# Kernel tuning notes

Measured on AMD Instinct MI355X. Metric: run time of the kernel, lower is better.

The kernel has to match this reference:

```python
import jax, jax.numpy as jnp
import numpy as np
from jax import lax

EPS = 1e-5
K = 32
S1, S2 = 512, 256


def bn_relu(x, gamma, beta, axes):
    # BatchNorm in training mode (batch statistics, biased variance) + ReLU.
    mean = jnp.mean(x, axis=axes, keepdims=True)
    var = jnp.var(x, axis=axes, keepdims=True)
    return jax.nn.relu((x - mean) * lax.rsqrt(var + EPS) * gamma + beta)


def fps(xyz, s):
    # Farthest point sampling, deterministic start at index 0. xyz: [N,3] -> [s] indices
    N = xyz.shape[0]
    def body(carry, _):
        dist, far = carry
        d = jnp.sum((xyz - xyz[far]) ** 2, axis=-1)
        dist = jnp.minimum(dist, d)
        return (dist, jnp.argmax(dist).astype(jnp.int32)), far
    init = (jnp.full((N,), 1e10, xyz.dtype), jnp.int32(0))
    _, idx = lax.scan(body, init, None, length=s)
    return idx


def sample_and_knn_group(s, k, coords, features):
    # coords: [B,N,3], features: [B,N,D]
    fps_idx = jax.vmap(lambda c: fps(c, s))(coords)                      # [B,s]
    new_xyz = jnp.take_along_axis(coords, fps_idx[..., None], axis=1)   # [B,s,3]
    new_feat = jnp.take_along_axis(features, fps_idx[..., None], axis=1)  # [B,s,D]
    # squared euclidean distances [B,s,N]
    d2 = (jnp.sum(new_xyz ** 2, -1)[..., None]
          - 2.0 * jnp.einsum('bsc,bnc->bsn', new_xyz, coords)
          + jnp.sum(coords ** 2, -1)[:, None, :])
    _, knn_idx = lax.top_k(-d2, k)                                       # [B,s,k]
    grouped = jax.vmap(lambda f, i: f[i])(features, knn_idx)             # [B,s,k,D]
    rel = grouped - new_feat[:, :, None, :]
    agg = jnp.concatenate([rel, jnp.broadcast_to(new_feat[:, :, None, :], rel.shape)], axis=-1)  # [B,s,k,2D]
    return new_xyz, agg


def sg_block(s, coords, feats, w1, cb1, g1, b1, w2, cb2, g2, b2):
    new_xyz, agg = sample_and_knn_group(s, K, coords, feats)
    h = bn_relu(jnp.einsum('bskc,oc->bsko', agg, w1) + cb1, g1, b1, (0, 1, 2))
    h = bn_relu(jnp.einsum('bskc,oc->bsko', h, w2) + cb2, g2, b2, (0, 1, 2))
    return new_xyz, jnp.max(h, axis=2)  # max over k neighbors -> [B,s,O]


def setup_inputs() -> dict:
    key = jax.random.key(0)
    ks = jax.random.split(key, 8)
    B, N = 16, 2048
    sc = 0.05
    return {
        'x': jax.random.normal(ks[0], (B, 3, N), jnp.float32),
        'emb_w1': jax.random.normal(ks[1], (64, 3), jnp.float32) * sc,
        'emb_g1': jnp.ones((64,), jnp.float32), 'emb_b1': jnp.zeros((64,), jnp.float32),
        'emb_w2': jax.random.normal(ks[2], (64, 64), jnp.float32) * sc,
        'emb_g2': jnp.ones((64,), jnp.float32), 'emb_b2': jnp.zeros((64,), jnp.float32),
        'sg1_w1': jax.random.normal(ks[3], (128, 128), jnp.float32) * sc,
        'sg1_cb1': jnp.zeros((128,), jnp.float32),
        'sg1_g1': jnp.ones((128,), jnp.float32), 'sg1_b1': jnp.zeros((128,), jnp.float32),
        'sg1_w2': jax.random.normal(ks[4], (128, 128), jnp.float32) * sc,
        'sg1_cb2': jnp.zeros((128,), jnp.float32),
        'sg1_g2': jnp.ones((128,), jnp.float32), 'sg1_b2': jnp.zeros((128,), jnp.float32),
        'sg2_w1': jax.random.normal(ks[5], (512, 256), jnp.float32) * sc,
        'sg2_cb1': jnp.zeros((512,), jnp.float32),
        'sg2_g1': jnp.ones((512,), jnp.float32), 'sg2_b1': jnp.zeros((512,), jnp.float32),
        'sg2_w2': jax.random.normal(ks[6], (512, 512), jnp.float32) * sc,
        'sg2_cb2': jnp.zeros((512,), jnp.float32),
        'sg2_g2': jnp.ones((512,), jnp.float32), 'sg2_b2': jnp.zeros((512,), jnp.float32),
    }


def reference(x, emb_w1, emb_g1, emb_b1, emb_w2, emb_g2, emb_b2,
              sg1_w1, sg1_cb1, sg1_g1, sg1_b1, sg1_w2, sg1_cb2, sg1_g2, sg1_b2,
              sg2_w1, sg2_cb1, sg2_g1, sg2_b1, sg2_w2, sg2_cb2, sg2_g2, sg2_b2):
    xyz = jnp.transpose(x, (0, 2, 1))  # [B,N,3]
    f = bn_relu(jnp.einsum('bnc,oc->bno', xyz, emb_w1), emb_g1, emb_b1, (0, 1))   # [B,N,64]
    f = bn_relu(jnp.einsum('bnc,oc->bno', f, emb_w2), emb_g2, emb_b2, (0, 1))
    xyz1, f1 = sg_block(S1, xyz, f, sg1_w1, sg1_cb1, sg1_g1, sg1_b1,
                        sg1_w2, sg1_cb2, sg1_g2, sg1_b2)   # [B,512,128]
    _, f2 = sg_block(S2, xyz1, f1, sg2_w1, sg2_cb1, sg2_g1, sg2_b1,
                     sg2_w2, sg2_cb2, sg2_g2, sg2_b2)      # [B,256,512]
    return jnp.transpose(f2, (0, 2, 1))  # [B,512,256] to match torch [B,C,s]
```

## Files before the change

kernel.cpp:

```cpp
#include <hip/hip_runtime.h>
#include <hip/hip_bf16.h>

#define EPS_BN 1e-5f
constexpr int BB = 16, NN = 2048, SS1 = 512, SS2 = 256, KNb = 32;

typedef short bf16x8 __attribute__((ext_vector_type(8)));
typedef float f32x4 __attribute__((ext_vector_type(4)));

__device__ inline float bflo(unsigned u) { return __uint_as_float(u << 16); }
__device__ inline float bfhi(unsigned u) { return __uint_as_float(u & 0xffff0000u); }
__device__ inline unsigned short f2bf_bits(float v) {
  __hip_bfloat16 h = __float2bfloat16(v);
  return *reinterpret_cast<unsigned short*>(&h);
}
__device__ inline unsigned fmono(float v) {
  int b = __float_as_int(v);
  return (unsigned)(b ^ ((b >> 31) | 0x80000000));
}
__device__ inline unsigned bn2(unsigned u, float s0, float h0, float s1, float h1) {
  float v0 = fmaxf(bflo(u) * s0 + h0, 0.f);
  float v1 = fmaxf(bfhi(u) * s1 + h1, 0.f);
  return (unsigned)f2bf_bits(v0) | ((unsigned)f2bf_bits(v1) << 16);
}

template <int CTRL>
__device__ inline void dpp_step_min(unsigned& hi, unsigned& lo) {
  unsigned hs = (unsigned)__builtin_amdgcn_update_dpp((int)hi, (int)hi, CTRL, 0xF, 0xF, false);
  unsigned ls = (unsigned)__builtin_amdgcn_update_dpp((int)lo, (int)lo, CTRL, 0xF, 0xF, false);
  bool take = (hs < hi) || (hs == hi && ls < lo);
  hi = take ? hs : hi; lo = take ? ls : lo;
}
template <int CTRL>
__device__ inline void dpp_step_maxv_minidx(unsigned& hi, unsigned& lo) {
  unsigned hs = (unsigned)__builtin_amdgcn_update_dpp((int)hi, (int)hi, CTRL, 0xF, 0xF, false);
  unsigned ls = (unsigned)__builtin_amdgcn_update_dpp((int)lo, (int)lo, CTRL, 0xF, 0xF, false);
  bool take = (hs > hi) || (hs == hi && ls < lo);
  hi = take ? hs : hi; lo = take ? ls : lo;
}
__device__ inline void dpp_chain_min(unsigned& hi, unsigned& lo) {
  dpp_step_min<0x111>(hi, lo); dpp_step_min<0x112>(hi, lo);
  dpp_step_min<0x114>(hi, lo); dpp_step_min<0x118>(hi, lo);
  dpp_step_min<0x142>(hi, lo); dpp_step_min<0x143>(hi, lo);
}
__device__ inline void dpp_chain_maxv_minidx(unsigned& hi, unsigned& lo) {
  dpp_step_maxv_minidx<0x111>(hi, lo); dpp_step_maxv_minidx<0x112>(hi, lo);
  dpp_step_maxv_minidx<0x114>(hi, lo); dpp_step_maxv_minidx<0x118>(hi, lo);
  dpp_step_maxv_minidx<0x142>(hi, lo); dpp_step_maxv_minidx<0x143>(hi, lo);
}
__device__ inline int dpp_reduce_min_idx(unsigned hi, unsigned lo) {
  dpp_chain_min(hi, lo);
  return __builtin_amdgcn_readlane((int)lo, 63);
}

__global__ __launch_bounds__(256, 1) void k_mega1(
    const float* __restrict__ x, const float* __restrict__ emb_w1,
    float* __restrict__ fA, double* __restrict__ rsE1, double* __restrict__ rqE1,
    int* __restrict__ fps1, float* __restrict__ nx1,
    int* __restrict__ fps2, float* __restrict__ nx2,
    const float* __restrict__ w11f, __hip_bfloat16* __restrict__ wb11,
    const float* __restrict__ w12f, __hip_bfloat16* __restrict__ wb12,
    const float* __restrict__ w21f, __hip_bfloat16* __restrict__ wb21,
    const float* __restrict__ w22f, __hip_bfloat16* __restrict__ wb22) {
  int blk = blockIdx.x;
  int t = threadIdx.x;
  if (blk < BB) {
    constexpr int PPL = NN / 256;
    int b = blk; int w = t >> 6; int lane = t & 63;
    __shared__ float4 sxyz[NN];
    __shared__ float4 c4[SS1];
    __shared__ unsigned combH[2][4], combL[2][4];
    float px[PPL], py[PPL], pz[PPL], ds[PPL];
#pragma unroll
    for (int r = 0; r < PPL; r++) {
      int i = r * 256 + t;
      float xx = x[(size_t)(b * 3 + 0) * NN + i];
      float yy = x[(size_t)(b * 3 + 1) * NN + i];
      float zz = x[(size_t)(b * 3 + 2) * NN + i];
      px[r] = xx; py[r] = yy; pz[r] = zz;
      float ox = xx, oy = yy, oz = zz;
      asm volatile("" : "+v"(ox), "+v"(oy), "+v"(oz));
      float4 o4 = {ox, oy, oz, 0.f};
      sxyz[i] = o4;
      ds[r] = 1e10f;
    }
    __syncthreads();
    int far = 0; int p = 0;
    for (int it = 0; it < SS1; it++) {
      float4 f4 = sxyz[far];
      float fx = f4.x, fy = f4.y, fz = f4.z;
      if (t == 0) {
        fps1[b * SS1 + it] = far;
        size_t ob = ((size_t)b * SS1 + it) * 3;
        nx1[ob] = fx; nx1[ob + 1] = fy; nx1[ob + 2] = fz;
        c4[it] = f4;
      }
      float mm0 = -1.f, mm1 = -1.f, mm2 = -1.f, mm3 = -1.f;
#pragma unroll
      for (int r = 0; r < PPL; r++) {
        float dx = px[r] - fx, dy = py[r] - fy, dz = pz[r] - fz;
        float d = dx * dx + dy * dy + dz * dz;
        float nd = d < ds[r] ? d : ds[r];
        ds[r] = nd;
        if ((r & 3) == 0) mm0 = nd > mm0 ? nd : mm0;
        else if ((r & 3) == 1) mm1 = nd > mm1 ? nd : mm1;
        else if ((r & 3) == 2) mm2 = nd > mm2 ? nd : mm2;
        else mm3 = nd > mm3 ? nd : mm3;
      }
      float m = fmaxf(fmaxf(mm0, mm1), fmaxf(mm2, mm3));
      int cand[PPL];
#pragma unroll
      for (int r = 0; r < PPL; r++) cand[r] = (ds[r] == m) ? (r * 256 + t) : 0x7fffffff;
#pragma unroll
      for (int st = PPL / 2; st > 0; st >>= 1)
#pragma unroll
        for (int r = 0; r < st; r++) cand[r] = cand[r] < cand[r + st] ? cand[r] : cand[r + st];
      unsigned hi = __float_as_uint(m);
      unsigned lo = (unsigned)cand[0];
      dpp_chain_maxv_minidx(hi, lo);
      unsigned rh = (unsigned)__builtin_amdgcn_readlane((int)hi, 63);
      unsigned rl = (unsigned)__builtin_amdgcn_readlane((int)lo, 63);
      if (lane == 0) { combH[p][w] = rh; combL[p][w] = rl; }
      __syncthreads();
      unsigned bh = combH[p][0], bl = combL[p][0];
#pragma unroll
      for (int ww = 1; ww < 4; ww++) {
        unsigned oh = combH[p][ww], ol = combL[p][ww];
        bool take = (oh > bh) || (oh == bh && ol < bl);
        bh = take ? oh : bh; bl = take ? ol : bl;
      }
      far = (int)bl;
      p ^= 1;
    }
    __syncthreads();
    if (t >= 64) return;
    float qx[8], qy[8], qz[8], es[8];
#pragma unroll
    for (int r = 0; r < 8; r++) {
      float4 v = c4[r * 64 + t];
      qx[r] = v.x; qy[r] = v.y; qz[r] = v.z; es[r] = 1e10f;
    }
    int far2 = 0;
    for (int it = 0; it < SS2; it++) {
      float4 f4 = c4[far2];
      float fx = f4.x, fy = f4.y, fz = f4.z;
      if (t == 0) {
        fps2[b * SS2 + it] = far2;
        size_t ob = ((size_t)b * SS2 + it) * 3;
        nx2[ob] = fx; nx2[ob + 1] = fy; nx2[ob + 2] = fz;
      }
      float mm0 = -1.f, mm1 = -1.f, mm2 = -1.f, mm3 = -1.f;
#pragma unroll
      for (int r = 0; r < 8; r++) {
        float dx = qx[r] - fx, dy = qy[r] - fy, dz = qz[r] - fz;
        float d = dx * dx + dy * dy + dz * dz;
        float nd = d < es[r] ? d : es[r];
        es[r] = nd;
        if ((r & 3) == 0) mm0 = nd > mm0 ? nd : mm0;
        else if ((r & 3) == 1) mm1 = nd > mm1 ? nd : mm1;
        else if ((r & 3) == 2) mm2 = nd > mm2 ? nd : mm2;
        else mm3 = nd > mm3 ? nd : mm3;
      }
      float m = fmaxf(fmaxf(mm0, mm1), fmaxf(mm2, mm3));
      int cand[8];
#pragma unroll
      for (int r = 0; r < 8; r++) cand[r] = (es[r] == m) ? (r * 64 + t) : 0x7fffffff;
#pragma unroll
      for (int st = 4; st > 0; st >>= 1)
#pragma unroll
        for (int r = 0; r < st; r++) cand[r] = cand[r] < cand[r + st] ? cand[r] : cand[r + st];
      unsigned hi = __float_as_uint(m), lo = (unsigned)cand[0];
      dpp_chain_maxv_minidx(hi, lo);
      far2 = __builtin_amdgcn_readlane((int)lo, 63);
    }
    return;
  }
  blk -= BB;
  if (blk < 8192) {
    __shared__ float ls[64], lq[64];
    if (t < 64) { ls[t] = 0.f; lq[t] = 0.f; }
    __syncthreads();
    int o = t & 63;
    int pt = blk * 4 + (t >> 6);
    int b = pt >> 11, n = pt & (NN - 1);
    float x0 = x[(size_t)(b * 3 + 0) * NN + n];
    float x1 = x[(size_t)(b * 3 + 1) * NN + n];
    float x2 = x[(size_t)(b * 3 + 2) * NN + n];
    float v = x0 * emb_w1[o * 3] + x1 * emb_w1[o * 3 + 1] + x2 * emb_w1[o * 3 + 2];
    fA[(size_t)pt * 64 + o] = v;
    atomicAdd(&ls[o], v);
    atomicAdd(&lq[o], v * v);
    __syncthreads();
    if (t < 64) {
      int rep = blk & 63;
      atomicAdd(&rsE1[(size_t)rep * 64 + t], (double)ls[t]);
      atomicAdd(&rqE1[(size_t)rep * 64 + t], (double)lq[t]);
    }
    return;
  }
  blk -= 8192;
  if (blk < 64) { int i = blk * 256 + t; wb11[i] = __float2bfloat16(w11f[i]); return; }
  blk -= 64;
  if (blk < 64) { int i = blk * 256 + t; wb12[i] = __float2bfloat16(w12f[i]); return; }
  blk -= 64;
  if (blk < 512) { int i = blk * 256 + t; wb21[i] = __float2bfloat16(w21f[i]); return; }
  blk -= 512;
  { int i = blk * 256 + t; wb22[i] = __float2bfloat16(w22f[i]); }
}

__global__ __launch_bounds__(256) void k_mega2(
    const float* __restrict__ x, const float* __restrict__ nx1, int* __restrict__ knn1,
    const float* __restrict__ nx2, int* __restrict__ knn2,
    const float* __restrict__ fA, const float* __restrict__ sce1,
    const float* __restrict__ she1, const float* __restrict__ w2,
    float* __restrict__ fB, double* __restrict__ rsE2, double* __restrict__ rqE2) {
  int blk = blockIdx.x; int t = threadIdx.x;
  if (blk < 2048) {
    constexpr int PPL = NN / 64;
    int lane = t & 63;
    int center = blk * 4 + (t >> 6);
    int b = center >> 9;
    float cx = nx1[(size_t)center * 3], cy = nx1[(size_t)center * 3 + 1],
          cz = nx1[(size_t)center * 3 + 2];
    float cn = cx * cx + cy * cy + cz * cz;
    float d2[PPL];
#pragma unroll
    for (int r = 0; r < PPL; r++) {
      int i = r * 64 + lane;
      float xx = x[(size_t)(b * 3 + 0) * NN + i];
      float yy = x[(size_t)(b * 3 + 1) * NN + i];
      float zz = x[(size_t)(b * 3 + 2) * NN + i];
      d2[r] = cn - 2.f * (cx * xx + cy * yy + cz * zz) + (xx * xx + yy * yy + zz * zz);
    }
    for (int kk = 0; kk < KNb; kk++) {
      float a0 = d2[0], a1 = d2[1], a2 = d2[2], a3 = d2[3];
#pragma unroll
      for (int r = 4; r < PPL; r += 4) {
        a0 = fminf(a0, d2[r]); a1 = fminf(a1, d2[r + 1]);
        a2 = fminf(a2, d2[r + 2]); a3 = fminf(a3, d2[r + 3]);
      }
      float m = fminf(fminf(a0, a1), fminf(a2, a3));
      int cand[PPL];
#pragma unroll
      for (int r = 0; r < PPL; r++) cand[r] = (d2[r] == m) ? (r * 64 + lane) : 0x7fffffff;
#pragma unroll
      for (int st = PPL / 2; st > 0; st >>= 1)
#pragma unroll
        for (int r = 0; r < st; r++) cand[r] = cand[r] < cand[r + st] ? cand[r] : cand[r + st];
      int widx = dpp_reduce_min_idx(fmono(m), (unsigned)cand[0]);
      if (lane == 0) knn1[(size_t)center * KNb + kk] = widx;
      int wr = widx >> 6, wl = widx & 63;
#pragma unroll
      for (int r = 0; r < PPL; r++) d2[r] = (r == wr && lane == wl) ? 3.4e38f : d2[r];
    }
    return;
  }
  blk -= 2048;
  if (blk < 1024) {
    constexpr int PPL = SS1 / 64;
    int lane = t & 63;
    int center = blk * 4 + (t >> 6);
    int b = center >> 8;
    float cx = nx2[(size_t)center * 3], cy = nx2[(size_t)center * 3 + 1],
          cz = nx2[(size_t)center * 3 + 2];
    float cn = cx * cx + cy * cy + cz * cz;
    float d2[PPL];
#pragma unroll
    for (int r = 0; r < PPL; r++) {
      int i = r * 64 + lane;
      size_t pb = ((size_t)b * SS1 + i) * 3;
      float xx = nx1[pb], yy = nx1[pb + 1], zz = nx1[pb + 2];
      d2[r] = cn - 2.f * (cx * xx + cy * yy + cz * zz) + (xx * xx + yy * yy + zz * zz);
    }
    for (int kk = 0; kk < KNb; kk++) {
      float a0 = d2[0], a1 = d2[1], a2 = d2[2], a3 = d2[3];
      a0 = fminf(a0, d2[4]); a1 = fminf(a1, d2[5]);
      a2 = fminf(a2, d2[6]); a3 = fminf(a3, d2[7]);
      float m = fminf(fminf(a0, a1), fminf(a2, a3));
      int cand[PPL];
#pragma unroll
      for (int r = 0; r < PPL; r++) cand[r] = (d2[r] == m) ? (r * 64 + lane) : 0x7fffffff;
#pragma unroll
      for (int st = PPL / 2; st > 0; st >>= 1)
#pragma unroll
        for (int r = 0; r < st; r++) cand[r] = cand[r] < cand[r + st] ? cand[r] : cand[r + st];
      int widx = dpp_reduce_min_idx(fmono(m), (unsigned)cand[0]);
      if (lane == 0) knn2[(size_t)center * KNb + kk] = widx;
      int wr = widx >> 6, wl = widx & 63;
#pragma unroll
      for (int r = 0; r < PPL; r++) d2[r] = (r == wr && lane == wl) ? 3.4e38f : d2[r];
    }
    return;
  }
  blk -= 1024;
  __shared__ float wT[64][65];
  __shared__ float fs[16][64];
  __shared__ float ss[64], sq[64];
#pragma unroll
  for (int k = 0; k < 16; k++) {
    int idx = k * 256 + t;
    wT[idx & 63][idx >> 6] = w2[idx];
  }
  if (t < 64) { ss[t] = 0.f; sq[t] = 0.f; }
  int pt0 = blk * 16;
#pragma unroll
  for (int it = 0; it < 4; it++) {
    int idx = it * 256 + t;
    int p = idx >> 6, c = idx & 63;
    float v = fA[(size_t)(pt0 + p) * 64 + c];
    v = fmaxf(v * sce1[c] + she1[c], 0.f);
    fs[p][c] = v;
  }
  __syncthreads();
#pragma unroll
  for (int it = 0; it < 4; it++) {
    int idx = it * 256 + t;
    int p = idx >> 6, o = idx & 63;
    float acc = 0.f;
#pragma unroll 8
    for (int c = 0; c < 64; c++) acc += fs[p][c] * wT[c][o];
    fB[(size_t)(pt0 + p) * 64 + o] = acc;
    atomicAdd(&ss[o], acc);
    atomicAdd(&sq[o], acc * acc);
  }
  __syncthreads();
  if (t < 64) {
    int rep = blk & 63;
    atomicAdd(&rsE2[(size_t)rep * 64 + t], (double)ss[t]);
    atomicAdd(&rqE2[(size_t)rep * 64 + t], (double)sq[t]);
  }
}

template <int D, bool BN>
__global__ __launch_bounds__(256) void k_gather(const float* __restrict__ feat, int N,
                                                const int* __restrict__ fpsidx,
                                                const int* __restrict__ knn, int S,
                                                const float* __restrict__ bnsc,
                                                const float* __restrict__ bnsh,
                                                __hip_bfloat16* __restrict__ A) {
  int blk = blockIdx.x; int b = blk / S; int t = threadIdx.x;
  __shared__ float cf[D]; __shared__ int nbr[KNb];
  if (t < KNb) nbr[t] = knn[(size_t)blk * KNb + t];
  int center = fpsidx[blk];
  for (int c = t; c < D; c += 256) {
    float v = feat[((size_t)b * N + center) * D + c];
    if constexpr (BN) v = fmaxf(v * bnsc[c] + bnsh[c], 0.f);
    cf[c] = v;
  }
  __syncthreads();
  for (int i = t; i < KNb * D; i += 256) {
    int kk = i / D, c = i - kk * D;
    float v = feat[((size_t)b * N + nbr[kk]) * D + c];
    if constexpr (BN) v = fmaxf(v * bnsc[c] + bnsh[c], 0.f);
    size_t row = (size_t)blk * KNb + kk;
    A[row * (2 * D) + c] = __float2bfloat16(v - cf[c]);
    A[row * (2 * D) + D + c] = __float2bfloat16(cf[c]);
  }
}

__global__ __launch_bounds__(256) void k_gather_feat(
    const float* __restrict__ maxb, const float* __restrict__ minb,
    const float* __restrict__ sc, const float* __restrict__ sh,
    const int* __restrict__ fpsidx, const int* __restrict__ knn,
    __hip_bfloat16* __restrict__ A) {
  constexpr int D = 128;
  int blk = blockIdx.x; int b = blk / SS2; int t = threadIdx.x;
  __shared__ float cf[D]; __shared__ int nbr[KNb];
  if (t < KNb) nbr[t] = knn[(size_t)blk * KNb + t];
  int center = fpsidx[blk];
  for (int c = t; c < D; c += 256) {
    size_t row = (size_t)b * SS1 + center;
    float s = sc[c];
    float sel = s > 0.f ? maxb[row * D + c] : minb[row * D + c];
    cf[c] = fmaxf(sel * s + sh[c], 0.f);
  }
  __syncthreads();
  for (int i = t; i < KNb * D; i += 256) {
    int kk = i / D, c = i - kk * D;
    size_t row = (size_t)b * SS1 + nbr[kk];
    float s = sc[c];
    float sel = s > 0.f ? maxb[row * D + c] : minb[row * D + c];
    float v = fmaxf(sel * s + sh[c], 0.f);
    size_t orow = (size_t)blk * KNb + kk;
    A[orow * (2 * D) + c] = __float2bfloat16(v - cf[c]);
    A[orow * (2 * D) + D + c] = __float2bfloat16(cf[c]);
  }
}

template <int K, int EPI, bool BNA>
__global__ __launch_bounds__(256) void k_mgemm(
    const __hip_bfloat16* __restrict__ A, const __hip_bfloat16* __restrict__ W,
    int N, int Mtiles, const float* __restrict__ bias,
    const float* __restrict__ bnsc, const float* __restrict__ bnsh,
    __hip_bfloat16* __restrict__ Hout,
    float* __restrict__ maxb, float* __restrict__ minb,
    double* __restrict__ rsum, double* __restrict__ rsq) {
  constexpr int SP = 40;
  int bm = blockIdx.x % Mtiles; int bn = blockIdx.x / Mtiles;
  int t = threadIdx.x; int w = t >> 6; int lane = t & 63;
  int wm = w & 1, wn = w >> 1; int quad = lane >> 4; int l15 = lane & 15;
  __shared__ short As[128 * SP];
  __shared__ short Ws[128 * SP];
  __shared__ float scs[BNA ? K : 1], shs[BNA ? K : 1];
  if constexpr (BNA) {
    for (int i = t; i < K; i += 256) { scs[i] = bnsc[i]; shs[i] = bnsh[i]; }
  }
  f32x4 acc[4][4];
  f32x4 zero = {0.f, 0.f, 0.f, 0.f};
#pragma unroll
  for (int i = 0; i < 4; i++)
#pragma unroll
    for (int j = 0; j < 4; j++) acc[i][j] = zero;

  int srow = t >> 2, sseg = t & 3;
  const short* Ag = (const short*)A;
  const short* Wg = (const short*)W;
  size_t arow0 = (size_t)bm * 128;
  size_t wrow0 = (size_t)bn * 128;

  for (int k0 = 0; k0 < K; k0 += 32) {
    __syncthreads();
    uint4 a0 = *(const uint4*)(Ag + (arow0 + srow) * K + k0 + sseg * 8);
    uint4 a1 = *(const uint4*)(Ag + (arow0 + srow + 64) * K + k0 + sseg * 8);
    uint4 b0 = *(const uint4*)(Wg + (wrow0 + srow) * K + k0 + sseg * 8);
    uint4 b1 = *(const uint4*)(Wg + (wrow0 + srow + 64) * K + k0 + sseg * 8);
    if constexpr (BNA) {
      int cb = k0 + sseg * 8;
      float s[8], h[8];
#pragma unroll
      for (int q = 0; q < 8; q++) { s[q] = scs[cb + q]; h[q] = shs[cb + q]; }
      a0.x = bn2(a0.x, s[0], h[0], s[1], h[1]);
      a0.y = bn2(a0.y, s[2], h[2], s[3], h[3]);
      a0.z = bn2(a0.z, s[4], h[4], s[5], h[5]);
      a0.w = bn2(a0.w, s[6], h[6], s[7], h[7]);
      a1.x = bn2(a1.x, s[0], h[0], s[1], h[1]);
      a1.y = bn2(a1.y, s[2], h[2], s[3], h[3]);
      a1.z = bn2(a1.z, s[4], h[4], s[5], h[5]);
      a1.w = bn2(a1.w, s[6], h[6], s[7], h[7]);
    }
    *(uint4*)(As + srow * SP + sseg * 8) = a0;
    *(uint4*)(As + (srow + 64) * SP + sseg * 8) = a1;
    *(uint4*)(Ws + srow * SP + sseg * 8) = b0;
    *(uint4*)(Ws + (srow + 64) * SP + sseg * 8) = b1;
    __syncthreads();
    bf16x8 af[4], bfr[4];
#pragma unroll
    for (int i = 0; i < 4; i++)
      af[i] = *(const bf16x8*)(As + (wm * 64 + i * 16 + l15) * SP + quad * 8);
#pragma unroll
    for (int j = 0; j < 4; j++)
      bfr[j] = *(const bf16x8*)(Ws + (wn * 64 + j * 16 + l15) * SP + quad * 8);
#pragma unroll
    for (int i = 0; i < 4; i++)
#pragma unroll
      for (int j = 0; j < 4; j++)
        acc[i][j] = __builtin_amdgcn_mfma_f32_16x16x32_bf16(af[i], bfr[j], acc[i][j], 0, 0, 0);
  }

  if constexpr (EPI == 0) {
    int rep = blockIdx.x & 63;
#pragma unroll
    for (int j = 0; j < 4; j++) {
      int col = bn * 128 + wn * 64 + j * 16 + l15;
      float bs = bias[col];
      float su = 0.f, sq = 0.f;
#pragma unroll
      for (int i = 0; i < 4; i++)
#pragma unroll
        for (int r = 0; r < 4; r++) {
          int row = bm * 128 + wm * 64 + i * 16 + quad * 4 + r;
          float v = acc[i][j][r] + bs;
          Hout[(size_t)row * N + col] = __float2bfloat16(v);
          su += v; sq += v * v;
        }
      atomicAdd(&rsum[(size_t)rep * N + col], (double)su);
      atomicAdd(&rsq[(size_t)rep * N + col], (double)sq);
    }
  } else {
    __shared__ float buf[128][33];
    for (int s = 0; s < 4; s++) {
      __syncthreads();
      if (wn == (s >> 1)) {
        int jb = 2 * (s & 1);
#pragma unroll
        for (int jj = 0; jj < 2; jj++) {
          int j = jb + jj;
          int lcol = jj * 16 + l15;
          float bs = bias[bn * 128 + s * 32 + lcol];
#pragma unroll
          for (int i = 0; i < 4; i++)
#pragma unroll
            for (int r = 0; r < 4; r++)
              buf[wm * 64 + i * 16 + quad * 4 + r][lcol] = acc[i][j][r] + bs;
        }
      }
      __syncthreads();
      if (t < 128) {
        int g = t >> 5, c = t & 31;
        float mx = -3.4e38f, mn = 3.4e38f, su = 0.f, sq = 0.f;
#pragma unroll
        for (int r = 0; r < 32; r++) {
          float v = buf[g * 32 + r][c];
          mx = fmaxf(mx, v); mn = fminf(mn, v);
          su += v; sq += v * v;
        }
        int col = bn * 128 + s * 32 + c;
        size_t gidx = (size_t)bm * 4 + g;
        maxb[gidx * N + col] = mx;
        minb[gidx * N + col] = mn;
        int rep = blockIdx.x & 63;
        atomicAdd(&rsum[(size_t)rep * N + col], (double)su);
        atomicAdd(&rsq[(size_t)rep * N + col], (double)sq);
      }
    }
  }
}

__global__ void k_finalize(const double* __restrict__ rsum, const double* __restrict__ rsq,
                           int O, int rows,
                           const float* __restrict__ gamma, const float* __restrict__ beta,
                           float* __restrict__ scale, float* __restrict__ shift) {
  int o = blockIdx.x * blockDim.x + threadIdx.x;
  if (o >= O) return;
  double s = 0, s2 = 0;
  for (int r = 0; r < 64; r++) { s += rsum[(size_t)r * O + o]; s2 += rsq[(size_t)r * O + o]; }
  double mean = s / rows;
  double var = s2 / rows - mean * mean;
  float sc = gamma[o] * rsqrtf((float)var + EPS_BN);
  scale[o] = sc; shift[o] = beta[o] - (float)mean * sc;
}

__global__ void k_final_out(const float* __restrict__ maxb, const float* __restrict__ minb,
                            const float* __restrict__ scale, const float* __restrict__ shift,
                            float* __restrict__ out) {
  int idx = blockIdx.x * blockDim.x + threadIdx.x;
  if (idx >= BB * SS2 * 512) return;
  int o = idx % 512; int si = (idx / 512) % SS2; int b = idx / (512 * SS2);
  float sc = scale[o];
  float sel = sc > 0.f ? maxb[idx] : minb[idx];
  out[((size_t)b * 512 + o) * SS2 + si] = fmaxf(sel * sc + shift[o], 0.f);
}

extern "C" void kernel_launch(void* const* d_in, const int* in_sizes, int n_in,
                              void* d_out, int out_size, void* d_ws, size_t ws_size,
                              hipStream_t stream) {
  const float* x       = (const float*)d_in[0];
  const float* emb_w1  = (const float*)d_in[1];
  const float* emb_g1  = (const float*)d_in[2];
  const float* emb_b1  = (const float*)d_in[3];
  const float* emb_w2  = (const float*)d_in[4];
  const float* emb_g2  = (const float*)d_in[5];
  const float* emb_b2  = (const float*)d_in[6];
  const float* sg1_w1  = (const float*)d_in[7];
  const float* sg1_cb1 = (const float*)d_in[8];
  const float* sg1_g1  = (const float*)d_in[9];
  const float* sg1_b1  = (const float*)d_in[10];
  const float* sg1_w2  = (const float*)d_in[11];
  const float* sg1_cb2 = (const float*)d_in[12];
  const float* sg1_g2  = (const float*)d_in[13];
  const float* sg1_b2  = (const float*)d_in[14];
  const float* sg2_w1  = (const float*)d_in[15];
  const float* sg2_cb1 = (const float*)d_in[16];
  const float* sg2_g1  = (const float*)d_in[17];
  const float* sg2_b1  = (const float*)d_in[18];
  const float* sg2_w2  = (const float*)d_in[19];
  const float* sg2_cb2 = (const float*)d_in[20];
  const float* sg2_g2  = (const float*)d_in[21];
  const float* sg2_b2  = (const float*)d_in[22];

  char* ws = (char*)d_ws;
  size_t off = 0;
  auto alloc = [&](size_t bytes) -> size_t {
    size_t cur = off; off += (bytes + 255) & ~(size_t)255; return cur;
  };
  float* fA   = (float*)(ws + alloc((size_t)BB * NN * 64 * 4));
  float* fB   = (float*)(ws + alloc((size_t)BB * NN * 64 * 4));
  float* nx1  = (float*)(ws + alloc((size_t)BB * SS1 * 3 * 4));
  float* nx2  = (float*)(ws + alloc((size_t)BB * SS2 * 3 * 4));
  int* fps1   = (int*)(ws + alloc((size_t)BB * SS1 * 4));
  int* fps2   = (int*)(ws + alloc((size_t)BB * SS2 * 4));
  int* knn1   = (int*)(ws + alloc((size_t)BB * SS1 * KNb * 4));
  int* knn2   = (int*)(ws + alloc((size_t)BB * SS2 * KNb * 4));
  float* maxb = (float*)(ws + alloc((size_t)BB * SS2 * 512 * 4));
  float* minb = (float*)(ws + alloc((size_t)BB * SS2 * 512 * 4));
  float* scbuf = (float*)(ws + alloc((size_t)12 * 512 * 4));
  float* sc11 = scbuf + 4 * 512, *sh11 = scbuf + 5 * 512;
  float* sc12 = scbuf + 6 * 512, *sh12 = scbuf + 7 * 512;
  float* sc21 = scbuf + 8 * 512, *sh21 = scbuf + 9 * 512;
  float* sc22 = scbuf + 10 * 512, *sh22 = scbuf + 11 * 512;
  float* sc_e1 = scbuf + 0 * 512, *sh_e1 = scbuf + 1 * 512;
  float* sc_e2 = scbuf + 2 * 512, *sh_e2 = scbuf + 3 * 512;
  size_t statsz = (size_t)12 * 64 * 512 * 8;
  char* statz = ws + alloc(statsz);
  double* st = (double*)statz;
  double* rsA = st + 0 * 64 * 512, *rqA = st + 1 * 64 * 512;
  double* rsB = st + 2 * 64 * 512, *rqB = st + 3 * 64 * 512;
  double* rsC = st + 4 * 64 * 512, *rqC = st + 5 * 64 * 512;
  double* rsD = st + 6 * 64 * 512, *rqD = st + 7 * 64 * 512;
  double* rsE1 = st + 8 * 64 * 512, *rqE1 = st + 9 * 64 * 512;
  double* rsE2 = st + 10 * 64 * 512, *rqE2 = st + 11 * 64 * 512;
  __hip_bfloat16* wb11 = (__hip_bfloat16*)(ws + alloc(128 * 128 * 2));
  __hip_bfloat16* wb12 = (__hip_bfloat16*)(ws + alloc(128 * 128 * 2));
  __hip_bfloat16* wb21 = (__hip_bfloat16*)(ws + alloc(512 * 256 * 2));
  __hip_bfloat16* wb22 = (__hip_bfloat16*)(ws + alloc(512 * 512 * 2));
  __hip_bfloat16* Abuf = (__hip_bfloat16*)(ws + alloc((size_t)262144 * 128 * 2));
  __hip_bfloat16* Hbuf = (__hip_bfloat16*)(ws + alloc((size_t)131072 * 512 * 2));

  hipMemsetAsync(statz, 0, statsz, stream);

  const int thr = 256;
  k_mega1<<<9872, 256, 0, stream>>>(x, emb_w1, fA, rsE1, rqE1, fps1, nx1, fps2, nx2,
                                    sg1_w1, wb11, sg1_w2, wb12, sg2_w1, wb21, sg2_w2, wb22);
  k_finalize<<<1, 64, 0, stream>>>(rsE1, rqE1, 64, BB * NN, emb_g1, emb_b1, sc_e1, sh_e1);
  k_mega2<<<5120, 256, 0, stream>>>(x, nx1, knn1, nx2, knn2, fA, sc_e1, sh_e1, emb_w2,
                                    fB, rsE2, rqE2);
  k_finalize<<<1, 64, 0, stream>>>(rsE2, rqE2, 64, BB * NN, emb_g2, emb_b2, sc_e2, sh_e2);

  k_gather<64, true><<<BB * SS1, 256, 0, stream>>>(fB, NN, fps1, knn1, SS1,
                                                   sc_e2, sh_e2, Abuf);
  k_mgemm<128, 0, false><<<2048, 256, 0, stream>>>(Abuf, wb11, 128, 2048, sg1_cb1,
                                                   nullptr, nullptr, Hbuf,
                                                   nullptr, nullptr, rsA, rqA);
  k_finalize<<<1, 128, 0, stream>>>(rsA, rqA, 128, 262144, sg1_g1, sg1_b1, sc11, sh11);
  k_mgemm<128, 1, true><<<2048, 256, 0, stream>>>(Hbuf, wb12, 128, 2048, sg1_cb2,
                                                  sc11, sh11, nullptr,
                                                  maxb, minb, rsB, rqB);
  k_finalize<<<1, 128, 0, stream>>>(rsB, rqB, 128, 262144, sg1_g2, sg1_b2, sc12, sh12);

  k_gather_feat<<<BB * SS2, 256, 0, stream>>>(maxb, minb, sc12, sh12, fps2, knn2, Abuf);
  k_mgemm<256, 0, false><<<1024 * 4, 256, 0, stream>>>(Abuf, wb21, 512, 1024, sg2_cb1,
                                                       nullptr, nullptr, Hbuf,
                                                       nullptr, nullptr, rsC, rqC);
  k_finalize<<<4, 128, 0, stream>>>(rsC, rqC, 512, 131072, sg2_g1, sg2_b1, sc21, sh21);
  k_mgemm<512, 1, true><<<1024 * 4, 256, 0, stream>>>(Hbuf, wb22, 512, 1024, sg2_cb2,
                                                      sc21, sh21, nullptr,
                                                      maxb, minb, rsD, rqD);
  k_finalize<<<4, 128, 0, stream>>>(rsD, rqD, 512, 131072, sg2_g2, sg2_b2, sc22, sh22);
  k_final_out<<<(BB * SS2 * 512 + thr - 1) / thr, thr, 0, stream>>>(maxb, minb, sc22, sh22,
                                                                    (float*)d_out);
}
```

Measured before the change: 1.225 ms.

## Fuse kNN gather and relative-feature build into GEMM A-tile loads

Removes the standalone gather kernels that materialised the grouped [rel, center] bf16 matrix in global memory. The first GEMM of each set-abstraction block now reads neighbour features directly through the kNN indices and applies BN/ReLU (or max/min selection) on the fly. It subtracts the centre features cached in shared memory while filling the A tile. This saves a large write-then-read of the A buffer and two launches, but adds irregular gathered loads inside the GEMM loop. In the second block each A tile is recomputed once for every one of the four N tiles.

```diff
diff --git a/kernel.cpp b/kernel.cpp
--- a/kernel.cpp
+++ b/kernel.cpp
@@ -13,6 +13,9 @@
   __hip_bfloat16 h = __float2bfloat16(v);
   return *reinterpret_cast<unsigned short*>(&h);
 }
+__device__ inline unsigned packbf(float a, float b) {
+  return (unsigned)f2bf_bits(a) | ((unsigned)f2bf_bits(b) << 16);
+}
 __device__ inline unsigned fmono(float v) {
   int b = __float_as_int(v);
   return (unsigned)(b ^ ((b >> 31) | 0x80000000));
@@ -20,7 +23,7 @@
 __device__ inline unsigned bn2(unsigned u, float s0, float h0, float s1, float h1) {
   float v0 = fmaxf(bflo(u) * s0 + h0, 0.f);
   float v1 = fmaxf(bfhi(u) * s1 + h1, 0.f);
-  return (unsigned)f2bf_bits(v0) | ((unsigned)f2bf_bits(v1) << 16);
+  return packbf(v0, v1);
 }
 
 template <int CTRL>
@@ -330,79 +333,54 @@
   }
 }
 
-template <int D, bool BN>
-__global__ __launch_bounds__(256) void k_gather(const float* __restrict__ feat, int N,
-                                                const int* __restrict__ fpsidx,
-                                                const int* __restrict__ knn, int S,
-                                                const float* __restrict__ bnsc,
-                                                const float* __restrict__ bnsh,
-                                                __hip_bfloat16* __restrict__ A) {
-  int blk = blockIdx.x; int b = blk / S; int t = threadIdx.x;
-  __shared__ float cf[D]; __shared__ int nbr[KNb];
-  if (t < KNb) nbr[t] = knn[(size_t)blk * KNb + t];
-  int center = fpsidx[blk];
-  for (int c = t; c < D; c += 256) {
-    float v = feat[((size_t)b * N + center) * D + c];
-    if constexpr (BN) v = fmaxf(v * bnsc[c] + bnsh[c], 0.f);
-    cf[c] = v;
-  }
-  __syncthreads();
-  for (int i = t; i < KNb * D; i += 256) {
-    int kk = i / D, c = i - kk * D;
-    float v = feat[((size_t)b * N + nbr[kk]) * D + c];
-    if constexpr (BN) v = fmaxf(v * bnsc[c] + bnsh[c], 0.f);
-    size_t row = (size_t)blk * KNb + kk;
-    A[row * (2 * D) + c] = __float2bfloat16(v - cf[c]);
-    A[row * (2 * D) + D + c] = __float2bfloat16(cf[c]);
-  }
-}
-
-__global__ __launch_bounds__(256) void k_gather_feat(
-    const float* __restrict__ maxb, const float* __restrict__ minb,
-    const float* __restrict__ sc, const float* __restrict__ sh,
-    const int* __restrict__ fpsidx, const int* __restrict__ knn,
-    __hip_bfloat16* __restrict__ A) {
-  constexpr int D = 128;
-  int blk = blockIdx.x; int b = blk / SS2; int t = threadIdx.x;
-  __shared__ float cf[D]; __shared__ int nbr[KNb];
-  if (t < KNb) nbr[t] = knn[(size_t)blk * KNb + t];
-  int center = fpsidx[blk];
-  for (int c = t; c < D; c += 256) {
-    size_t row = (size_t)b * SS1 + center;
-    float s = sc[c];
-    float sel = s > 0.f ? maxb[row * D + c] : minb[row * D + c];
-    cf[c] = fmaxf(sel * s + sh[c], 0.f);
-  }
-  __syncthreads();
-  for (int i = t; i < KNb * D; i += 256) {
-    int kk = i / D, c = i - kk * D;
-    size_t row = (size_t)b * SS1 + nbr[kk];
-    float s = sc[c];
-    float sel = s > 0.f ? maxb[row * D + c] : minb[row * D + c];
-    float v = fmaxf(sel * s + sh[c], 0.f);
-    size_t orow = (size_t)blk * KNb + kk;
-    A[orow * (2 * D) + c] = __float2bfloat16(v - cf[c]);
-    A[orow * (2 * D) + D + c] = __float2bfloat16(cf[c]);
-  }
-}
-
-template <int K, int EPI, bool BNA>
+template <int K, int EPI, bool BNA, int GA>
 __global__ __launch_bounds__(256) void k_mgemm(
     const __hip_bfloat16* __restrict__ A, const __hip_bfloat16* __restrict__ W,
     int N, int Mtiles, const float* __restrict__ bias,
     const float* __restrict__ bnsc, const float* __restrict__ bnsh,
+    const float* __restrict__ gsrc0, const float* __restrict__ gsrc1,
+    const float* __restrict__ gsc, const float* __restrict__ gsh,
+    const int* __restrict__ gfps, const int* __restrict__ gknn,
     __hip_bfloat16* __restrict__ Hout,
     float* __restrict__ maxb, float* __restrict__ minb,
     double* __restrict__ rsum, double* __restrict__ rsq) {
   constexpr int SP = 40;
+  constexpr int D = K / 2;
   int bm = blockIdx.x % Mtiles; int bn = blockIdx.x / Mtiles;
   int t = threadIdx.x; int w = t >> 6; int lane = t & 63;
   int wm = w & 1, wn = w >> 1; int quad = lane >> 4; int l15 = lane & 15;
   __shared__ short As[128 * SP];
   __shared__ short Ws[128 * SP];
   __shared__ float scs[BNA ? K : 1], shs[BNA ? K : 1];
+  __shared__ int nbrs[GA ? 128 : 1];
+  __shared__ float cfs[GA ? 4 : 1][GA ? D : 1];
+  __shared__ float gscs[GA ? D : 1], gshs[GA ? D : 1];
+  __shared__ int bGs[4];
   if constexpr (BNA) {
     for (int i = t; i < K; i += 256) { scs[i] = bnsc[i]; shs[i] = bnsh[i]; }
+  }
+  if constexpr (GA > 0) {
+    constexpr int SDIV = (GA == 1) ? SS1 : SS2;
+    constexpr int SRCN = (GA == 1) ? NN : SS1;
+    if (t < 128) nbrs[t] = gknn[((size_t)bm * 4 + (t >> 5)) * KNb + (t & 31)];
+    for (int i = t; i < D; i += 256) { gscs[i] = gsc[i]; gshs[i] = gsh[i]; }
+    if (t < 4) bGs[t] = (bm * 4 + t) / SDIV;
+    for (int idx = t; idx < 4 * D; idx += 256) {
+      int g = idx / D, c = idx - g * D;
+      int cidx = bm * 4 + g;
+      int b_ = cidx / SDIV;
+      int ctr = gfps[cidx];
+      size_t rowb = ((size_t)b_ * SRCN + ctr) * D + c;
+      float s = gsc[c];
+      float v;
+      if constexpr (GA == 1) {
+        v = fmaxf(gsrc0[rowb] * s + gsh[c], 0.f);
+      } else {
+        float sel = s > 0.f ? gsrc0[rowb] : gsrc1[rowb];
+        v = fmaxf(sel * s + gsh[c], 0.f);
+      }
+      cfs[g][c] = v;
+    }
   }
   f32x4 acc[4][4];
   f32x4 zero = {0.f, 0.f, 0.f, 0.f};
@@ -419,24 +397,75 @@
 
   for (int k0 = 0; k0 < K; k0 += 32) {
     __syncthreads();
-    uint4 a0 = *(const uint4*)(Ag + (arow0 + srow) * K + k0 + sseg * 8);
-    uint4 a1 = *(const uint4*)(Ag + (arow0 + srow + 64) * K + k0 + sseg * 8);
+    uint4 a0, a1;
+    if constexpr (GA > 0) {
+      constexpr int SRCN = (GA == 1) ? NN : SS1;
+      int col0 = k0 + sseg * 8;
+      auto mk = [&](int row) -> uint4 {
+        int g = row >> 5;
+        unsigned o[4];
+        if (col0 < D) {
+          int nb = nbrs[row];
+          int b_ = bGs[g];
+          size_t base = ((size_t)b_ * SRCN + nb) * D + col0;
+          float wv[8];
+          if constexpr (GA == 1) {
+            float4 v0 = *(const float4*)(gsrc0 + base);
+            float4 v1 = *(const float4*)(gsrc0 + base + 4);
+            wv[0] = v0.x; wv[1] = v0.y; wv[2] = v0.z; wv[3] = v0.w;
+            wv[4] = v1.x; wv[5] = v1.y; wv[6] = v1.z; wv[7] = v1.w;
+#pragma unroll
+            for (int q = 0; q < 8; q++)
+              wv[q] = fmaxf(wv[q] * gscs[col0 + q] + gshs[col0 + q], 0.f);
+          } else {
+            float4 x0 = *(const float4*)(gsrc0 + base);
+            float4 x1 = *(const float4*)(gsrc0 + base + 4);
+            float4 n0 = *(const float4*)(gsrc1 + base);
+            float4 n1 = *(const float4*)(gsrc1 + base + 4);
+            float mx[8] = {x0.x, x0.y, x0.z, x0.w, x1.x, x1.y, x1.z, x1.w};
+            float mn[8] = {n0.x, n0.y, n0.z, n0.w, n1.x, n1.y, n1.z, n1.w};
+#pragma unroll
+            for (int q = 0; q < 8; q++) {
+              float s = gscs[col0 + q];
+              float sel = s > 0.f ? mx[q] : mn[q];
+              wv[q] = fmaxf(sel * s + gshs[col0 + q], 0.f);
+            }
+          }
+#pragma unroll
+          for (int q = 0; q < 4; q++)
+            o[q] = packbf(wv[2 * q] - cfs[g][col0 + 2 * q],
+                          wv[2 * q + 1] - cfs[g][col0 + 2 * q + 1]);
+        } else {
+          int c2 = col0 - D;
+#pragma unroll
+          for (int q = 0; q < 4; q++)
+            o[q] = packbf(cfs[g][c2 + 2 * q], cfs[g][c2 + 2 * q + 1]);
+        }
+        uint4 out = {o[0], o[1], o[2], o[3]};
+        return out;
+      };
+      a0 = mk(srow);
+      a1 = mk(srow + 64);
+    } else {
+      a0 = *(const uint4*)(Ag + (arow0 + srow) * K + k0 + sseg * 8);
+      a1 = *(const uint4*)(Ag + (arow0 + srow + 64) * K + k0 + sseg * 8);
+      if constexpr (BNA) {
+        int cb = k0 + sseg * 8;
+        float s[8], h[8];
+#pragma unroll
+        for (int q = 0; q < 8; q++) { s[q] = scs[cb + q]; h[q] = shs[cb + q]; }
+        a0.x = bn2(a0.x, s[0], h[0], s[1], h[1]);
+        a0.y = bn2(a0.y, s[2], h[2], s[3], h[3]);
+        a0.z = bn2(a0.z, s[4], h[4], s[5], h[5]);
+        a0.w = bn2(a0.w, s[6], h[6], s[7], h[7]);
+        a1.x = bn2(a1.x, s[0], h[0], s[1], h[1]);
+        a1.y = bn2(a1.y, s[2], h[2], s[3], h[3]);
+        a1.z = bn2(a1.z, s[4], h[4], s[5], h[5]);
+        a1.w = bn2(a1.w, s[6], h[6], s[7], h[7]);
+      }
+    }
     uint4 b0 = *(const uint4*)(Wg + (wrow0 + srow) * K + k0 + sseg * 8);
     uint4 b1 = *(const uint4*)(Wg + (wrow0 + srow + 64) * K + k0 + sseg * 8);
-    if constexpr (BNA) {
-      int cb = k0 + sseg * 8;
-      float s[8], h[8];
-#pragma unroll
-      for (int q = 0; q < 8; q++) { s[q] = scs[cb + q]; h[q] = shs[cb + q]; }
-      a0.x = bn2(a0.x, s[0], h[0], s[1], h[1]);
-      a0.y = bn2(a0.y, s[2], h[2], s[3], h[3]);
-      a0.z = bn2(a0.z, s[4], h[4], s[5], h[5]);
-      a0.w = bn2(a0.w, s[6], h[6], s[7], h[7]);
-      a1.x = bn2(a1.x, s[0], h[0], s[1], h[1]);
-      a1.y = bn2(a1.y, s[2], h[2], s[3], h[3]);
-      a1.z = bn2(a1.z, s[4], h[4], s[5], h[5]);
-      a1.w = bn2(a1.w, s[6], h[6], s[7], h[7]);
-    }
     *(uint4*)(As + srow * SP + sseg * 8) = a0;
     *(uint4*)(As + (srow + 64) * SP + sseg * 8) = a1;
     *(uint4*)(Ws + srow * SP + sseg * 8) = b0;
@@ -602,7 +631,6 @@
   __hip_bfloat16* wb12 = (__hip_bfloat16*)(ws + alloc(128 * 128 * 2));
   __hip_bfloat16* wb21 = (__hip_bfloat16*)(ws + alloc(512 * 256 * 2));
   __hip_bfloat16* wb22 = (__hip_bfloat16*)(ws + alloc(512 * 512 * 2));
-  __hip_bfloat16* Abuf = (__hip_bfloat16*)(ws + alloc((size_t)262144 * 128 * 2));
   __hip_bfloat16* Hbuf = (__hip_bfloat16*)(ws + alloc((size_t)131072 * 512 * 2));
 
   hipMemsetAsync(statz, 0, statsz, stream);
@@ -615,25 +643,26 @@
                                     fB, rsE2, rqE2);
   k_finalize<<<1, 64, 0, stream>>>(rsE2, rqE2, 64, BB * NN, emb_g2, emb_b2, sc_e2, sh_e2);
 
-  k_gather<64, true><<<BB * SS1, 256, 0, stream>>>(fB, NN, fps1, knn1, SS1,
-                                                   sc_e2, sh_e2, Abuf);
-  k_mgemm<128, 0, false><<<2048, 256, 0, stream>>>(Abuf, wb11, 128, 2048, sg1_cb1,
-                                                   nullptr, nullptr, Hbuf,
-                                                   nullptr, nullptr, rsA, rqA);
+  k_mgemm<128, 0, false, 1><<<2048, 256, 0, stream>>>(
+      nullptr, wb11, 128, 2048, sg1_cb1, nullptr, nullptr,
+      fB, nullptr, sc_e2, sh_e2, fps1, knn1,
+      Hbuf, nullptr, nullptr, rsA, rqA);
   k_finalize<<<1, 128, 0, stream>>>(rsA, rqA, 128, 262144, sg1_g1, sg1_b1, sc11, sh11);
-  k_mgemm<128, 1, true><<<2048, 256, 0, stream>>>(Hbuf, wb12, 128, 2048, sg1_cb2,
-                                                  sc11, sh11, nullptr,
-                                                  maxb, minb, rsB, rqB);
+  k_mgemm<128, 1, true, 0><<<2048, 256, 0, stream>>>(
+      Hbuf, wb12, 128, 2048, sg1_cb2, sc11, sh11,
+      nullptr, nullptr, nullptr, nullptr, nullptr, nullptr,
+      nullptr, maxb, minb, rsB, rqB);
   k_finalize<<<1, 128, 0, stream>>>(rsB, rqB, 128, 262144, sg1_g2, sg1_b2, sc12, sh12);
 
-  k_gather_feat<<<BB * SS2, 256, 0, stream>>>(maxb, minb, sc12, sh12, fps2, knn2, Abuf);
-  k_mgemm<256, 0, false><<<1024 * 4, 256, 0, stream>>>(Abuf, wb21, 512, 1024, sg2_cb1,
-                                                       nullptr, nullptr, Hbuf,
-                                                       nullptr, nullptr, rsC, rqC);
+  k_mgemm<256, 0, false, 2><<<1024 * 4, 256, 0, stream>>>(
+      nullptr, wb21, 512, 1024, sg2_cb1, nullptr, nullptr,
+      maxb, minb, sc12, sh12, fps2, knn2,
+      Hbuf, nullptr, nullptr, rsC, rqC);
   k_finalize<<<4, 128, 0, stream>>>(rsC, rqC, 512, 131072, sg2_g1, sg2_b1, sc21, sh21);
-  k_mgemm<512, 1, true><<<1024 * 4, 256, 0, stream>>>(Hbuf, wb22, 512, 1024, sg2_cb2,
-                                                      sc21, sh21, nullptr,
-                                                      maxb, minb, rsD, rqD);
+  k_mgemm<512, 1, true, 0><<<1024 * 4, 256, 0, stream>>>(
+      Hbuf, wb22, 512, 1024, sg2_cb2, sc21, sh21,
+      nullptr, nullptr, nullptr, nullptr, nullptr, nullptr,
+      nullptr, maxb, minb, rsD, rqD);
   k_finalize<<<4, 128, 0, stream>>>(rsD, rqD, 512, 131072, sg2_g2, sg2_b2, sc22, sh22);
   k_final_out<<<(BB * SS2 * 512 + thr - 1) / thr, thr, 0, stream>>>(maxb, minb, sc22, sh22,
                                                                     (float*)d_out);
```

New measurement: 1.210 ms, median of 2. About the same (-1.2%).
